# Optimization experiments

Measured on AMD Instinct MI355X. Metric: run time of the kernel, lower is better.

The kernel has to match this reference:

```python
import jax, jax.numpy as jnp
import numpy as np

HEADS = 4
KNN_K = 20
BN_EPS = 1e-5


def conv1x1(w, b, x):
    # 1x1 Conv1d: w [out, in], x [B, in, N] -> [B, out, N]
    return jnp.einsum('oc,bcn->bon', w, x) + b[None, :, None]


def setup_inputs() -> dict:
    key = jax.random.key(0)
    B, C, N = 2, 128, 2048
    ks = jax.random.split(key, 16)
    W = lambda k, o, i: jax.random.normal(k, (o, i), jnp.float32) * 0.05
    V = lambda k, o: jax.random.normal(k, (o,), jnp.float32) * 0.05
    return {
        'desc1': jax.random.normal(ks[0], (B, C, N, 1), jnp.float32),
        'wq': W(ks[1], C, C), 'bq': V(ks[2], C),
        'wk': W(ks[3], C, C), 'bk': V(ks[4], C),
        'wv': W(ks[5], C, C), 'bv': V(ks[6], C),
        'wm': W(ks[7], C, C), 'bm': V(ks[8], C),
        'w1': W(ks[9], 2 * C, 2 * C), 'b1': V(ks[10], 2 * C),
        'gamma': jnp.ones((2 * C,), jnp.float32),
        'beta': jnp.zeros((2 * C,), jnp.float32),
        'w2': W(ks[11], C, 2 * C), 'b2': V(ks[12], C),
    }


def reference(desc1, wq, bq, wk, bk, wv, bv, wm, bm, w1, b1, gamma, beta, w2, b2):
    x = desc1[..., 0]                      # [B, C, N]
    B, C, N = x.shape
    D = C // HEADS

    q = conv1x1(wq, bq, x).reshape(B, HEADS, D, N)
    k = conv1x1(wk, bk, x).reshape(B, HEADS, D, N)
    v = conv1x1(wv, bv, x).reshape(B, HEADS, D, N)

    # kNN on raw descriptors: pd = -||xi||^2 + 2 xi.xj - ||xj||^2 (larger = closer)
    xx = jnp.sum(x * x, axis=1)            # [B, N]
    pd = 2.0 * jnp.einsum('bcn,bcm->bnm', x, x) - xx[:, :, None] - xx[:, None, :]
    idx = jax.lax.top_k(pd, KNN_K)[1]      # [B, N, K]

    # scatter ones at kNN indices, then keep only mutual neighbors
    bI = jnp.arange(B)[:, None, None]
    nI = jnp.arange(N)[None, :, None]
    mask = jnp.zeros((B, N, N), x.dtype).at[bI, nI, idx].set(1.0)
    mask = mask * mask.transpose(0, 2, 1)  # [B, N, N]

    score = jnp.einsum('bhdn,bhdm->bhnm', q, k) / (D ** 0.5)
    m = mask[:, None]                      # broadcast over heads
    score = score * m + (-1e9) * (1.0 - m)
    score = jax.nn.softmax(score, axis=-1)

    av = jnp.einsum('bhnm,bhdm->bhdn', score, v).reshape(B, C, N)
    av = conv1x1(wm, bm, av)

    h = conv1x1(w1, b1, jnp.concatenate([x, av], axis=1))  # [B, 2C, N]
    mu = jnp.mean(h, axis=(0, 2), keepdims=True)
    var = jnp.var(h, axis=(0, 2), keepdims=True)           # biased, matches torch BN
    h = (h - mu) / jnp.sqrt(var + BN_EPS) * gamma[None, :, None] + beta[None, :, None]
    h = jax.nn.relu(h)

    out = x + conv1x1(w2, b2, h)
    return out[..., None]                  # [B, C, N, 1]
```

## Files before the change

### kernel.cpp

```cpp
#include <hip/hip_runtime.h>
#include <math.h>

#define NPT 2048
#define KNN 20

typedef const float* fp;
typedef __attribute__((ext_vector_type(4))) float f32x4;
typedef __attribute__((ext_vector_type(8))) short s16x8;

__device__ __forceinline__ ushort f2bf_rne(float v) {
    unsigned u = __float_as_uint(v);
    unsigned r = u + 0x7FFFu + ((u >> 16) & 1u);
    return (ushort)(r >> 16);
}
__device__ __forceinline__ float bfbits2f(ushort h) {
    return __uint_as_float(((unsigned)h) << 16);
}
__device__ __forceinline__ s16x8 ldfrag(const ushort* p) {
    union { uint4 u; s16x8 s; } cv;
    cv.u = *reinterpret_cast<const uint4*>(p);
    return cv.s;
}
__device__ __forceinline__ void f8_hilo(const float* row, s16x8* hi, s16x8* lo) {
    float4 f0 = *reinterpret_cast<const float4*>(row);
    float4 f1 = *reinterpret_cast<const float4*>(row + 4);
    float f[8] = {f0.x, f0.y, f0.z, f0.w, f1.x, f1.y, f1.z, f1.w};
    union { ushort u[8]; s16x8 s; } H, L;
    #pragma unroll
    for (int j = 0; j < 8; j++) {
        ushort h = f2bf_rne(f[j]);
        H.u[j] = h;
        L.u[j] = f2bf_rne(f[j] - bfbits2f(h));
    }
    *hi = H.s; *lo = L.s;
}

__global__ __launch_bounds__(256) void prep_all(
    fp xbf, fp wq, fp wk, fp wv, fp wm, fp w1, fp w2, fp bm, fp b1,
    float* xx, ushort* xhiF, ushort* xloF,
    ushort* wqFhi, ushort* wqFlo, ushort* wkFhi, ushort* wkFlo,
    ushort* wvFhi, ushort* wvFlo,
    ushort* wcFhi, ushort* wcFlo, ushort* w2Fhi, ushort* w2Flo,
    float* b1p, float* stats) {
    int t = threadIdx.x;
    if (blockIdx.x < 256) {
        __shared__ float xs[16][129];
        __shared__ float xpart[16][17];
        int p0 = blockIdx.x * 16;
        int b = p0 >> 11, n0 = p0 & 2047;
        fp xb = xbf + (size_t)b * 128 * NPT;
        {
            int c = t >> 1, half = t & 1;
            float4 f0 = *reinterpret_cast<const float4*>(xb + (size_t)c * NPT + n0 + half * 8);
            float4 f1 = *reinterpret_cast<const float4*>(xb + (size_t)c * NPT + n0 + half * 8 + 4);
            xs[half * 8 + 0][c] = f0.x; xs[half * 8 + 1][c] = f0.y;
            xs[half * 8 + 2][c] = f0.z; xs[half * 8 + 3][c] = f0.w;
            xs[half * 8 + 4][c] = f1.x; xs[half * 8 + 5][c] = f1.y;
            xs[half * 8 + 6][c] = f1.z; xs[half * 8 + 7][c] = f1.w;
        }
        __syncthreads();
        int p = t & 15, g = t >> 4, c0 = g * 8;
        float f[8];
        #pragma unroll
        for (int j = 0; j < 8; j++) f[j] = xs[p][c0 + j];
        float ps = 0.f;
        #pragma unroll
        for (int j = 0; j < 8; j++) ps += f[j] * f[j];
        xpart[p][g] = ps;
        union { ushort u[8]; uint4 q; } H, L;
        #pragma unroll
        for (int j = 0; j < 8; j++) {
            ushort hi = f2bf_rne(f[j]);
            H.u[j] = hi;
            L.u[j] = f2bf_rne(f[j] - bfbits2f(hi));
        }
        size_t off = ((size_t)blockIdx.x * 4 + (c0 >> 5)) * 512
                   + (size_t)(((((c0 >> 3) & 3) * 16) + p) * 8);
        *reinterpret_cast<uint4*>(xhiF + off) = H.q;
        *reinterpret_cast<uint4*>(xloF + off) = L.q;
        __syncthreads();
        if (t < 16) {
            float s = 0.f;
            #pragma unroll
            for (int gg = 0; gg < 16; gg++) s += xpart[t][gg];
            xx[p0 + t] = s;
        }
        return;
    }
    int wid = (blockIdx.x - 256) * 256 + t;
    if (wid < 49152) {
        int which = wid >> 14, e = wid & 16383;
        int lane = (e >> 3) & 63, j = e & 7, kk = (e >> 9) & 3, nt = e >> 11;
        int n = nt * 16 + (lane & 15);
        int k = kk * 32 + (lane >> 4) * 8 + j;
        fp src = which == 0 ? wq : which == 1 ? wk : wv;
        float v = src[n * 128 + k];
        ushort hi = f2bf_rne(v);
        (which == 0 ? wqFhi : which == 1 ? wkFhi : wvFhi)[e] = hi;
        (which == 0 ? wqFlo : which == 1 ? wkFlo : wvFlo)[e] = f2bf_rne(v - bfbits2f(hi));
    } else if (wid < 114688) {
        int e = wid - 49152;
        int j = e & 7, lane = (e >> 3) & 63, kk = (e >> 9) & 7, nt = e >> 12;
        int n = nt * 16 + (lane & 15);
        int k = kk * 32 + (lane >> 4) * 8 + j;
        float v;
        if (k < 128) {
            v = w1[n * 256 + k];
        } else {
            int c = k - 128;
            float s = 0.f;
            for (int i = 0; i < 128; i += 4) {
                float4 wr = *reinterpret_cast<const float4*>(w1 + n * 256 + 128 + i);
                s += wr.x * wm[(i + 0) * 128 + c];
                s += wr.y * wm[(i + 1) * 128 + c];
                s += wr.z * wm[(i + 2) * 128 + c];
                s += wr.w * wm[(i + 3) * 128 + c];
            }
            v = s;
        }
        ushort hi = f2bf_rne(v);
        wcFhi[e] = hi;
        wcFlo[e] = f2bf_rne(v - bfbits2f(hi));
    } else if (wid < 147456) {
        int e = wid - 114688;
        int j = e & 7, lane = (e >> 3) & 63, kk = (e >> 9) & 7, nt = e >> 12;
        int n = nt * 16 + (lane & 15);
        int k = kk * 32 + (lane >> 4) * 8 + j;
        float v = w2[n * 256 + k];
        ushort hi = f2bf_rne(v);
        w2Fhi[e] = hi;
        w2Flo[e] = f2bf_rne(v - bfbits2f(hi));
    } else if (wid < 147712) {
        int o = wid - 147456;
        float s = b1[o];
        for (int i = 0; i < 128; i++)
            s += w1[o * 256 + 128 + i] * bm[i];
        b1p[o] = s;
    } else {
        stats[wid - 147712] = 0.0f;
    }
}

#define MERGE(off) { float ov = __shfl_xor(bv, off); int oi = __shfl_xor(bi, off); \
                     if (ov > bv || (ov == bv && oi < bi)) { bv = ov; bi = oi; } }

__global__ __launch_bounds__(1024) void gemm_key_topk(
    const ushort* xhiF, const ushort* xloF, const float* xx,
    const ushort* wqFhi, const ushort* wqFlo,
    const ushort* wkFhi, const ushort* wkFlo,
    const ushort* wvFhi, const ushort* wvFlo,
    fp bq, fp bk, fp bv_, float* qT, float* kT, float* vT,
    int* idxbuf, float* scratch) {
    __shared__ float chm[16][64];
    __shared__ float sv[16][256];
    __shared__ int   si[16][256];
    __shared__ float Trow[16];
    __shared__ int   rowcnt[16];
    __shared__ int   ovfAll;
    int tt = threadIdx.x, w = tt >> 6, lane = tt & 63;
    int rt = blockIdx.x;
    int slab = rt >> 7, rtl = rt & 127;
    int cl = lane & 15, quad = lane >> 4;

    if (tt < 16) rowcnt[tt] = 0;
    if (tt == 16) ovfAll = 0;

    s16x8 ahi[4], alo[4];
    #pragma unroll
    for (int kk = 0; kk < 4; kk++) {
        ahi[kk] = ldfrag(xhiF + ((size_t)(rt * 4 + kk)) * 512 + lane * 8);
        alo[kk] = ldfrag(xloF + ((size_t)(rt * 4 + kk)) * 512 + lane * 8);
    }

    if (w < 12) {
        f32x4 acc[2];
        acc[0] = (f32x4){0.f, 0.f, 0.f, 0.f};
        acc[1] = (f32x4){0.f, 0.f, 0.f, 0.f};
        #pragma unroll
        for (int kk = 0; kk < 4; kk++) {
            #pragma unroll
            for (int i = 0; i < 2; i++) {
                int pair = w * 2 + i;
                int mat = pair >> 3, nt = pair & 7;
                const ushort* whi = mat == 0 ? wqFhi : mat == 1 ? wkFhi : wvFhi;
                const ushort* wlo = mat == 0 ? wqFlo : mat == 1 ? wkFlo : wvFlo;
                s16x8 bhi = ldfrag(whi + ((size_t)(nt * 4 + kk)) * 512 + lane * 8);
                s16x8 blo = ldfrag(wlo + ((size_t)(nt * 4 + kk)) * 512 + lane * 8);
                acc[i] = __builtin_amdgcn_mfma_f32_16x16x32_bf16(ahi[kk], bhi, acc[i], 0, 0, 0);
                acc[i] = __builtin_amdgcn_mfma_f32_16x16x32_bf16(alo[kk], bhi, acc[i], 0, 0, 0);
                acc[i] = __builtin_amdgcn_mfma_f32_16x16x32_bf16(ahi[kk], blo, acc[i], 0, 0, 0);
            }
        }
        int p0 = rt * 16;
        #pragma unroll
        for (int i = 0; i < 2; i++) {
            int pair = w * 2 + i;
            int mat = pair >> 3, nt = pair & 7;
            fp bias    = mat == 0 ? bq : mat == 1 ? bk : bv_;
            float* out = mat == 0 ? qT : mat == 1 ? kT : vT;
            int o = nt * 16 + cl;
            float bvv = bias[o];
            #pragma unroll
            for (int r = 0; r < 4; r++)
                out[(size_t)(p0 + quad * 4 + r) * 128 + o] = acc[i][r] + bvv;
        }
    }

    f32x4 key[8];
    #pragma unroll
    for (int c = 0; c < 8; c++) {
        int ctl = w * 8 + c;
        int ct = slab * 128 + ctl;
        f32x4 a = (f32x4){0.f, 0.f, 0.f, 0.f};
        #pragma unroll
        for (int kk = 0; kk < 4; kk++) {
            s16x8 bh = ldfrag(xhiF + ((size_t)(ct * 4 + kk)) * 512 + lane * 8);
            s16x8 bl = ldfrag(xloF + ((size_t)(ct * 4 + kk)) * 512 + lane * 8);
            a = __builtin_amdgcn_mfma_f32_16x16x32_bf16(ahi[kk], bh, a, 0, 0, 0);
            a = __builtin_amdgcn_mfma_f32_16x16x32_bf16(alo[kk], bh, a, 0, 0, 0);
            a = __builtin_amdgcn_mfma_f32_16x16x32_bf16(ahi[kk], bl, a, 0, 0, 0);
        }
        float xxc = xx[slab * 2048 + ctl * 16 + cl];
        #pragma unroll
        for (int r = 0; r < 4; r++) a[r] = 2.0f * a[r] - xxc;
        key[c] = a;
    }

    {
        float m[4];
        #pragma unroll
        for (int r = 0; r < 4; r++) {
            float mm = key[0][r];
            #pragma unroll
            for (int c = 1; c < 8; c++) mm = fmaxf(mm, key[c][r]);
            mm = fmaxf(mm, __shfl_xor(mm, 1));
            mm = fmaxf(mm, __shfl_xor(mm, 2));
            m[r] = mm;
        }
        if ((cl & 3) == 0) {
            #pragma unroll
            for (int r = 0; r < 4; r++)
                chm[quad * 4 + r][w * 4 + (cl >> 2)] = m[r];
        }
    }
    __syncthreads();

    {
        float bs = chm[w][lane];
        #pragma unroll
        for (int k = 2; k <= 64; k <<= 1) {
            #pragma unroll
            for (int j = k >> 1; j > 0; j >>= 1) {
                float o = __shfl_xor(bs, j);
                bool dirDesc = (lane & k) != 0;
                bool upper   = (lane & j) != 0;
                bs = (upper != dirDesc) ? fmaxf(bs, o) : fminf(bs, o);
            }
        }
        float T = __shfl(bs, 44);
        if (lane == 0) Trow[w] = T;
    }
    __syncthreads();

    #pragma unroll
    for (int r = 0; r < 4; r++) {
        int row = quad * 4 + r;
        float T = Trow[row];
        #pragma unroll
        for (int c = 0; c < 8; c++) {
            float v = key[c][r];
            if (v >= T) {
                int pos = atomicAdd(&rowcnt[row], 1);
                if (pos < 256) {
                    sv[row][pos] = v;
                    si[row][pos] = w * 128 + c * 16 + cl;
                }
            }
        }
    }
    __syncthreads();
    if (tt == 0) {
        int o = 0;
        for (int i = 0; i < 16; i++) o |= (rowcnt[i] > 256) ? 1 : 0;
        ovfAll = o;
    }
    __syncthreads();
    int ovf = ovfAll;

    int S = rowcnt[w];
    if (S <= 256) {
        float vl[4]; int il[4];
        #pragma unroll
        for (int s = 0; s < 4; s++) {
            int g = lane + s * 64;
            bool ok = g < S;
            vl[s] = ok ? sv[w][g] : -3.4e38f;
            il[s] = ok ? si[w][g] : 0x7FFFFFFF;
        }
        unsigned removed = 0u;
        for (int iter = 0; iter < KNN; iter++) {
            float bv = -3.4e38f; int bi = 0x7FFFFFFF;
            #pragma unroll
            for (int s = 0; s < 4; s++) {
                bool live = ((removed >> s) & 1u) == 0u;
                if (live && (vl[s] > bv || (vl[s] == bv && il[s] < bi))) {
                    bv = vl[s]; bi = il[s];
                }
            }
            MERGE(32) MERGE(16) MERGE(8) MERGE(4) MERGE(2) MERGE(1)
            if (lane == 0)
                idxbuf[(size_t)(slab * 2048 + rtl * 16 + w) * KNN + iter] = bi & 2047;
            #pragma unroll
            for (int s = 0; s < 4; s++)
                if (il[s] == bi) removed |= 1u << s;
        }
    }

    if (ovf) {
        #pragma unroll
        for (int c = 0; c < 8; c++)
            #pragma unroll
            for (int r = 0; r < 4; r++)
                scratch[((size_t)rt * 16 + quad * 4 + r) * 2048 + w * 128 + c * 16 + cl]
                    = key[c][r];
        __syncthreads();
        if (rowcnt[w] > 256) {
            const float* rowp = scratch + ((size_t)rt * 16 + w) * 2048;
            float rv[32];
            #pragma unroll
            for (int j = 0; j < 32; j++) rv[j] = rowp[j * 64 + lane];
            unsigned removed = 0u;
            for (int iter = 0; iter < KNN; iter++) {
                float bv = -3.4e38f; int bi = 0;
                #pragma unroll
                for (int sl = 0; sl < 32; sl++) {
                    bool live = ((removed >> sl) & 1u) == 0u;
                    if (live && rv[sl] > bv) { bv = rv[sl]; bi = sl * 64 + lane; }
                }
                MERGE(32) MERGE(16) MERGE(8) MERGE(4) MERGE(2) MERGE(1)
                if (lane == 0)
                    idxbuf[(size_t)(slab * 2048 + rtl * 16 + w) * KNN + iter] = bi;
                if ((bi & 63) == lane) removed |= 1u << (bi >> 6);
            }
        }
    }
}

__global__ __launch_bounds__(256) void k3_attn(
    fp qT, fp kT, fp vT, const int* idxbuf, float* avT) {
    __shared__ float sbuf[2][KNN * 4];
    __shared__ int   mlist[2][KNN];
    __shared__ int   cnt_s[2];
    int tt = threadIdx.x;
    int half = tt >> 7, t = tt & 127;
    int p = blockIdx.x * 2 + half;
    int b = p >> 11, n = p & 2047;
    int bbase = b * NPT;
    int h = t >> 5;

    if ((tt >> 6) == half * 2) {
        int lane = tt & 63;
        bool fl = false; int m = 0;
        if (lane < KNN) {
            m = idxbuf[(size_t)p * KNN + lane] & 2047;
            const int4* mrow = reinterpret_cast<const int4*>(idxbuf + (size_t)(bbase + m) * KNN);
            int4 r0 = mrow[0], r1 = mrow[1], r2 = mrow[2], r3 = mrow[3], r4 = mrow[4];
            fl = (r0.x == n) || (r0.y == n) || (r0.z == n) || (r0.w == n)
              || (r1.x == n) || (r1.y == n) || (r1.z == n) || (r1.w == n)
              || (r2.x == n) || (r2.y == n) || (r2.z == n) || (r2.w == n)
              || (r3.x == n) || (r3.y == n) || (r3.z == n) || (r3.w == n)
              || (r4.x == n) || (r4.y == n) || (r4.z == n) || (r4.w == n);
        }
        unsigned long long mask = __ballot(fl);
        int pos = __popcll(mask & ((1ull << lane) - 1ull));
        if (fl) mlist[half][pos] = m;
        if (lane == 0) cnt_s[half] = (int)__popcll(mask);
    }
    __syncthreads();

    int cnt = cnt_s[half];
    float qv = qT[(size_t)p * 128 + t];
    for (int jj = 0; jj < cnt; jj++) {
        int m = mlist[half][jj];
        float prod = qv * kT[(size_t)(bbase + m) * 128 + t];
        prod += __shfl_xor(prod, 16);
        prod += __shfl_xor(prod, 8);
        prod += __shfl_xor(prod, 4);
        prod += __shfl_xor(prod, 2);
        prod += __shfl_xor(prod, 1);
        if ((t & 31) == 0) sbuf[half][jj * 4 + h] = prod * 0.17677669529663687f;
    }
    __syncthreads();

    float mx = -3.4e38f;
    for (int j = 0; j < cnt; j++) mx = fmaxf(mx, sbuf[half][j * 4 + h]);
    float den = 0.f;
    for (int j = 0; j < cnt; j++) den += expf(sbuf[half][j * 4 + h] - mx);
    float inv = (cnt > 0) ? (1.0f / den) : 0.0f;
    float acc = 0.f;
    for (int j = 0; j < cnt; j++) {
        float pw = expf(sbuf[half][j * 4 + h] - mx) * inv;
        acc += pw * vT[(size_t)(bbase + mlist[half][j]) * 128 + t];
    }
    avT[(size_t)p * 128 + t] = acc;
}

__global__ __launch_bounds__(256) void k4b_h(
    const ushort* xhiF, const ushort* xloF, const float* avT,
    const ushort* wcFhi, const ushort* wcFlo,
    const float* b1p, float* hbuf, float* stats) {
    int t = threadIdx.x, cs = t >> 6, lane = t & 63;
    int rt = blockIdx.x;
    int p0 = rt * 16;

    f32x4 acc[4];
    #pragma unroll
    for (int j = 0; j < 4; j++) acc[j] = (f32x4){0.f, 0.f, 0.f, 0.f};

    for (int kk = 0; kk < 8; kk++) {
        s16x8 ahi, alo;
        if (kk < 4) {
            ahi = ldfrag(xhiF + ((size_t)(rt * 4 + kk)) * 512 + lane * 8);
            alo = ldfrag(xloF + ((size_t)(rt * 4 + kk)) * 512 + lane * 8);
        } else {
            const float* arow = avT + (size_t)(p0 + (lane & 15)) * 128
                              + (kk - 4) * 32 + (lane >> 4) * 8;
            f8_hilo(arow, &ahi, &alo);
        }
        #pragma unroll
        for (int j = 0; j < 4; j++) {
            int nt = cs * 4 + j;
            s16x8 bhi = ldfrag(wcFhi + ((size_t)(nt * 8 + kk)) * 512 + lane * 8);
            s16x8 blo = ldfrag(wcFlo + ((size_t)(nt * 8 + kk)) * 512 + lane * 8);
            acc[j] = __builtin_amdgcn_mfma_f32_16x16x32_bf16(ahi, bhi, acc[j], 0, 0, 0);
            acc[j] = __builtin_amdgcn_mfma_f32_16x16x32_bf16(alo, bhi, acc[j], 0, 0, 0);
            acc[j] = __builtin_amdgcn_mfma_f32_16x16x32_bf16(ahi, blo, acc[j], 0, 0, 0);
        }
    }

    int cl = lane & 15, quad = lane >> 4;
    #pragma unroll
    for (int j = 0; j < 4; j++) {
        int o = cs * 64 + j * 16 + cl;
        float bb = b1p[o];
        float s = 0.f, s2 = 0.f;
        #pragma unroll
        for (int r = 0; r < 4; r++) {
            float v = acc[j][r] + bb;
            hbuf[(size_t)(p0 + quad * 4 + r) * 256 + o] = v;
            s += v; s2 += v * v;
        }
        s  += __shfl_xor(s, 16);  s  += __shfl_xor(s, 32);
        s2 += __shfl_xor(s2, 16); s2 += __shfl_xor(s2, 32);
        if (quad == 0) {
            atomicAdd(&stats[o], s);
            atomicAdd(&stats[256 + o], s2);
        }
    }
}

__global__ __launch_bounds__(256) void k5b_out(
    const float* hbuf, const float* stats, fp gamma, fp beta,
    const ushort* w2Fhi, const ushort* w2Flo,
    fp b2, fp xbf, float* out) {
    int t = threadIdx.x, wvi = t >> 6, lane = t & 63;
    int rt = blockIdx.x;
    int p0 = rt * 16;

    f32x4 acc[2];
    acc[0] = (f32x4){0.f, 0.f, 0.f, 0.f};
    acc[1] = (f32x4){0.f, 0.f, 0.f, 0.f};

    for (int kk = 0; kk < 8; kk++) {
        int c0 = kk * 32 + (lane >> 4) * 8;
        const float* hrow = hbuf + (size_t)(p0 + (lane & 15)) * 256 + c0;
        float4 f0 = *reinterpret_cast<const float4*>(hrow);
        float4 f1 = *reinterpret_cast<const float4*>(hrow + 4);
        float4 s0 = *reinterpret_cast<const float4*>(stats + c0);
        float4 s1 = *reinterpret_cast<const float4*>(stats + c0 + 4);
        float4 q0 = *reinterpret_cast<const float4*>(stats + 256 + c0);
        float4 q1 = *reinterpret_cast<const float4*>(stats + 256 + c0 + 4);
        float4 g0 = *reinterpret_cast<const float4*>(gamma + c0);
        float4 g1 = *reinterpret_cast<const float4*>(gamma + c0 + 4);
        float4 e0 = *reinterpret_cast<const float4*>(beta + c0);
        float4 e1 = *reinterpret_cast<const float4*>(beta + c0 + 4);
        float f[8] = {f0.x, f0.y, f0.z, f0.w, f1.x, f1.y, f1.z, f1.w};
        float sm[8] = {s0.x, s0.y, s0.z, s0.w, s1.x, s1.y, s1.z, s1.w};
        float sq[8] = {q0.x, q0.y, q0.z, q0.w, q1.x, q1.y, q1.z, q1.w};
        float gm[8] = {g0.x, g0.y, g0.z, g0.w, g1.x, g1.y, g1.z, g1.w};
        float bt[8] = {e0.x, e0.y, e0.z, e0.w, e1.x, e1.y, e1.z, e1.w};
        union { ushort u[8]; s16x8 s; } H, L;
        #pragma unroll
        for (int j = 0; j < 8; j++) {
            float mu  = sm[j] * (1.0f / 4096.0f);
            float var = fmaxf(sq[j] * (1.0f / 4096.0f) - mu * mu, 0.0f);
            float a    = gm[j] / sqrtf(var + 1e-5f);
            float cadd = bt[j] - mu * a;
            float v = fmaxf(f[j] * a + cadd, 0.0f);
            ushort hi = f2bf_rne(v);
            H.u[j] = hi;
            L.u[j] = f2bf_rne(v - bfbits2f(hi));
        }
        s16x8 ahi = H.s, alo = L.s;
        #pragma unroll
        for (int jj = 0; jj < 2; jj++) {
            int nt = wvi * 2 + jj;
            s16x8 bhi = ldfrag(w2Fhi + ((size_t)(nt * 8 + kk)) * 512 + lane * 8);
            s16x8 blo = ldfrag(w2Flo + ((size_t)(nt * 8 + kk)) * 512 + lane * 8);
            acc[jj] = __builtin_amdgcn_mfma_f32_16x16x32_bf16(ahi, bhi, acc[jj], 0, 0, 0);
            acc[jj] = __builtin_amdgcn_mfma_f32_16x16x32_bf16(alo, bhi, acc[jj], 0, 0, 0);
            acc[jj] = __builtin_amdgcn_mfma_f32_16x16x32_bf16(ahi, blo, acc[jj], 0, 0, 0);
        }
    }
    int cl = lane & 15, quad = lane >> 4;
    int b = p0 >> 11, n0 = p0 & 2047;
    #pragma unroll
    for (int jj = 0; jj < 2; jj++) {
        int o = (wvi * 2 + jj) * 16 + cl;
        float bb = b2[o];
        size_t base = (size_t)b * 128 * NPT + (size_t)o * NPT + n0 + quad * 4;
        float4 xv = *reinterpret_cast<const float4*>(xbf + base);
        float4 ov;
        ov.x = acc[jj][0] + bb + xv.x;
        ov.y = acc[jj][1] + bb + xv.y;
        ov.z = acc[jj][2] + bb + xv.z;
        ov.w = acc[jj][3] + bb + xv.w;
        *reinterpret_cast<float4*>(out + base) = ov;
    }
}

#define WS_FULL 44978176u

extern "C" void kernel_launch(void* const* d_in, const int* in_sizes, int n_in,
                              void* d_out, int out_size, void* d_ws, size_t ws_size,
                              hipStream_t stream) {
    fp desc1 = (fp)d_in[0];
    fp wq = (fp)d_in[1];  fp bq = (fp)d_in[2];
    fp wk = (fp)d_in[3];  fp bk = (fp)d_in[4];
    fp wv = (fp)d_in[5];  fp bv = (fp)d_in[6];
    fp wm = (fp)d_in[7];  fp bm = (fp)d_in[8];
    fp w1 = (fp)d_in[9];  fp b1 = (fp)d_in[10];
    fp gamma = (fp)d_in[11]; fp beta = (fp)d_in[12];
    fp w2 = (fp)d_in[13]; fp b2 = (fp)d_in[14];

    if (ws_size < (size_t)WS_FULL) return;

    char* ws = (char*)d_ws;
    float*  qT    = (float*) (ws + 0);
    float*  kT    = (float*) (ws + 2097152);
    float*  vT    = (float*) (ws + 4194304);
    float*  avT   = (float*) (ws + 6291456);
    float*  xx    = (float*) (ws + 8388608);
    int*    idxb  = (int*)   (ws + 8404992);
    float*  stats = (float*) (ws + 8732672);
    float*  b1p   = (float*) (ws + 8734720);
    ushort* wqFhi = (ushort*)(ws + 8736768);
    ushort* wqFlo = (ushort*)(ws + 8769536);
    ushort* wkFhi = (ushort*)(ws + 8802304);
    ushort* wkFlo = (ushort*)(ws + 8835072);
    ushort* wvFhi = (ushort*)(ws + 8867840);
    ushort* wvFlo = (ushort*)(ws + 8900608);
    ushort* wcFhi = (ushort*)(ws + 8933376);
    ushort* wcFlo = (ushort*)(ws + 9064448);
    ushort* w2Fhi = (ushort*)(ws + 9195520);
    ushort* w2Flo = (ushort*)(ws + 9261056);
    ushort* xhiF  = (ushort*)(ws + 9326592);
    ushort* xloF  = (ushort*)(ws + 10375168);
    float*  scratch = (float*)(ws + 11423744);
    float*  hbuf  = (float*) (ws + 0);

    prep_all<<<835, 256, 0, stream>>>(desc1, wq, wk, wv, wm, w1, w2, bm, b1,
                                      xx, xhiF, xloF,
                                      wqFhi, wqFlo, wkFhi, wkFlo, wvFhi, wvFlo,
                                      wcFhi, wcFlo, w2Fhi, w2Flo, b1p, stats);
    gemm_key_topk<<<256, 1024, 0, stream>>>(xhiF, xloF, xx,
                                            wqFhi, wqFlo, wkFhi, wkFlo,
                                            wvFhi, wvFlo,
                                            bq, bk, bv, qT, kT, vT, idxb,
                                            scratch);
    k3_attn<<<2048, 256, 0, stream>>>(qT, kT, vT, idxb, avT);
    k4b_h<<<256, 256, 0, stream>>>(xhiF, xloF, avT, wcFhi, wcFlo,
                                   b1p, hbuf, stats);
    k5b_out<<<256, 256, 0, stream>>>(hbuf, stats, gamma, beta, w2Fhi, w2Flo,
                                     b2, desc1, (float*)d_out);
}
```

Measured before the change: 187.0 us.

## Split kNN top-k columns across two blocks and merge partial lists

Measured after the change: 236.5 us. 26.4% more time.

```diff
diff --git a/kernel.cpp b/kernel.cpp
--- a/kernel.cpp
+++ b/kernel.cpp
@@ -144,26 +144,25 @@
 #define MERGE(off) { float ov = __shfl_xor(bv, off); int oi = __shfl_xor(bi, off); \
                      if (ov > bv || (ov == bv && oi < bi)) { bv = ov; bi = oi; } }
 
-__global__ __launch_bounds__(1024) void gemm_key_topk(
+__global__ __launch_bounds__(1024, 8) void gemm_key_topk(
     const ushort* xhiF, const ushort* xloF, const float* xx,
     const ushort* wqFhi, const ushort* wqFlo,
     const ushort* wkFhi, const ushort* wkFlo,
     const ushort* wvFhi, const ushort* wvFlo,
     fp bq, fp bk, fp bv_, float* qT, float* kT, float* vT,
-    int* idxbuf, float* scratch) {
-    __shared__ float chm[16][64];
+    float* pv, int* pi, float* scratch) {
+    __shared__ float chm[16][32];
     __shared__ float sv[16][256];
     __shared__ int   si[16][256];
     __shared__ float Trow[16];
     __shared__ int   rowcnt[16];
     __shared__ int   ovfAll;
     int tt = threadIdx.x, w = tt >> 6, lane = tt & 63;
-    int rt = blockIdx.x;
+    int rt = blockIdx.x >> 1, half = blockIdx.x & 1;
     int slab = rt >> 7, rtl = rt & 127;
     int cl = lane & 15, quad = lane >> 4;
 
     if (tt < 16) rowcnt[tt] = 0;
-    if (tt == 16) ovfAll = 0;
 
     s16x8 ahi[4], alo[4];
     #pragma unroll
@@ -172,7 +171,7 @@
         alo[kk] = ldfrag(xloF + ((size_t)(rt * 4 + kk)) * 512 + lane * 8);
     }
 
-    if (w < 12) {
+    if (half == 0 && w < 12) {
         f32x4 acc[2];
         acc[0] = (f32x4){0.f, 0.f, 0.f, 0.f};
         acc[1] = (f32x4){0.f, 0.f, 0.f, 0.f};
@@ -206,10 +205,10 @@
         }
     }
 
-    f32x4 key[8];
-    #pragma unroll
-    for (int c = 0; c < 8; c++) {
-        int ctl = w * 8 + c;
+    f32x4 key[4];
+    #pragma unroll
+    for (int c = 0; c < 4; c++) {
+        int ctl = half * 64 + w * 4 + c;
         int ct = slab * 128 + ctl;
         f32x4 a = (f32x4){0.f, 0.f, 0.f, 0.f};
         #pragma unroll
@@ -232,21 +231,22 @@
         for (int r = 0; r < 4; r++) {
             float mm = key[0][r];
             #pragma unroll
-            for (int c = 1; c < 8; c++) mm = fmaxf(mm, key[c][r]);
+            for (int c = 1; c < 4; c++) mm = fmaxf(mm, key[c][r]);
             mm = fmaxf(mm, __shfl_xor(mm, 1));
             mm = fmaxf(mm, __shfl_xor(mm, 2));
+            mm = fmaxf(mm, __shfl_xor(mm, 4));
             m[r] = mm;
         }
-        if ((cl & 3) == 0) {
+        if ((cl & 7) == 0) {
             #pragma unroll
             for (int r = 0; r < 4; r++)
-                chm[quad * 4 + r][w * 4 + (cl >> 2)] = m[r];
+                chm[quad * 4 + r][w * 2 + (cl >> 3)] = m[r];
         }
     }
     __syncthreads();
 
     {
-        float bs = chm[w][lane];
+        float bs = (lane < 32) ? chm[w][lane] : -3.4e38f;
         #pragma unroll
         for (int k = 2; k <= 64; k <<= 1) {
             #pragma unroll
@@ -267,13 +267,13 @@
         int row = quad * 4 + r;
         float T = Trow[row];
         #pragma unroll
-        for (int c = 0; c < 8; c++) {
+        for (int c = 0; c < 4; c++) {
             float v = key[c][r];
             if (v >= T) {
                 int pos = atomicAdd(&rowcnt[row], 1);
                 if (pos < 256) {
                     sv[row][pos] = v;
-                    si[row][pos] = w * 128 + c * 16 + cl;
+                    si[row][pos] = (half * 64 + w * 4 + c) * 16 + cl;
                 }
             }
         }
@@ -288,6 +288,7 @@
     int ovf = ovfAll;
 
     int S = rowcnt[w];
+    size_t obase = ((size_t)(slab * 2048 + rtl * 16 + w) * 2 + half) * KNN;
     if (S <= 256) {
         float vl[4]; int il[4];
         #pragma unroll
@@ -308,8 +309,7 @@
                 }
             }
             MERGE(32) MERGE(16) MERGE(8) MERGE(4) MERGE(2) MERGE(1)
-            if (lane == 0)
-                idxbuf[(size_t)(slab * 2048 + rtl * 16 + w) * KNN + iter] = bi & 2047;
+            if (lane == 0) { pv[obase + iter] = bv; pi[obase + iter] = bi & 2047; }
             #pragma unroll
             for (int s = 0; s < 4; s++)
                 if (il[s] == bi) removed |= 1u << s;
@@ -318,31 +318,48 @@
 
     if (ovf) {
         #pragma unroll
-        for (int c = 0; c < 8; c++)
+        for (int c = 0; c < 4; c++)
             #pragma unroll
             for (int r = 0; r < 4; r++)
-                scratch[((size_t)rt * 16 + quad * 4 + r) * 2048 + w * 128 + c * 16 + cl]
-                    = key[c][r];
+                scratch[((size_t)rt * 16 + quad * 4 + r) * 2048
+                        + (half * 64 + w * 4 + c) * 16 + cl] = key[c][r];
         __syncthreads();
         if (rowcnt[w] > 256) {
-            const float* rowp = scratch + ((size_t)rt * 16 + w) * 2048;
-            float rv[32];
-            #pragma unroll
-            for (int j = 0; j < 32; j++) rv[j] = rowp[j * 64 + lane];
+            const float* rowp = scratch + ((size_t)rt * 16 + w) * 2048 + half * 1024;
+            float rv[16];
+            #pragma unroll
+            for (int j = 0; j < 16; j++) rv[j] = rowp[j * 64 + lane];
             unsigned removed = 0u;
             for (int iter = 0; iter < KNN; iter++) {
                 float bv = -3.4e38f; int bi = 0;
                 #pragma unroll
-                for (int sl = 0; sl < 32; sl++) {
+                for (int sl = 0; sl < 16; sl++) {
                     bool live = ((removed >> sl) & 1u) == 0u;
-                    if (live && rv[sl] > bv) { bv = rv[sl]; bi = sl * 64 + lane; }
+                    if (live && rv[sl] > bv) {
+                        bv = rv[sl]; bi = half * 1024 + sl * 64 + lane;
+                    }
                 }
                 MERGE(32) MERGE(16) MERGE(8) MERGE(4) MERGE(2) MERGE(1)
-                if (lane == 0)
-                    idxbuf[(size_t)(slab * 2048 + rtl * 16 + w) * KNN + iter] = bi;
-                if ((bi & 63) == lane) removed |= 1u << (bi >> 6);
+                if (lane == 0) { pv[obase + iter] = bv; pi[obase + iter] = bi; }
+                if ((bi & 63) == lane) removed |= 1u << ((bi - half * 1024) >> 6);
             }
         }
+    }
+}
+
+__global__ __launch_bounds__(256) void merge_topk(
+    const float* pv, const int* pi, int* idxbuf) {
+    int row = blockIdx.x * 256 + threadIdx.x;
+    const float* va = pv + (size_t)row * 2 * KNN;
+    const int*   ia = pi + (size_t)row * 2 * KNN;
+    int a = 0, b = KNN;
+    #pragma unroll
+    for (int i = 0; i < KNN; i++) {
+        float x = va[a], y = va[b];
+        int ix = ia[a], iy = ia[b];
+        bool ta = (x > y) || (x == y && ix < iy);
+        idxbuf[(size_t)row * KNN + i] = ta ? ix : iy;
+        if (ta) a++; else b++;
     }
 }
 
@@ -529,7 +546,7 @@
     }
 }
 
-#define WS_FULL 44978176u
+#define WS_FULL 46288896u
 
 extern "C" void kernel_launch(void* const* d_in, const int* in_sizes, int n_in,
                               void* d_out, int out_size, void* d_ws, size_t ws_size,
@@ -566,18 +583,21 @@
     ushort* w2Flo = (ushort*)(ws + 9261056);
     ushort* xhiF  = (ushort*)(ws + 9326592);
     ushort* xloF  = (ushort*)(ws + 10375168);
-    float*  scratch = (float*)(ws + 11423744);
+    float*  pv    = (float*) (ws + 11423744);
+    int*    pi    = (int*)   (ws + 12079104);
+    float*  scratch = (float*)(ws + 12734464);
     float*  hbuf  = (float*) (ws + 0);
 
     prep_all<<<835, 256, 0, stream>>>(desc1, wq, wk, wv, wm, w1, w2, bm, b1,
                                       xx, xhiF, xloF,
                                       wqFhi, wqFlo, wkFhi, wkFlo, wvFhi, wvFlo,
                                       wcFhi, wcFlo, w2Fhi, w2Flo, b1p, stats);
-    gemm_key_topk<<<256, 1024, 0, stream>>>(xhiF, xloF, xx,
+    gemm_key_topk<<<512, 1024, 0, stream>>>(xhiF, xloF, xx,
                                             wqFhi, wqFlo, wkFhi, wkFlo,
                                             wvFhi, wvFlo,
-                                            bq, bk, bv, qT, kT, vT, idxb,
-                                            scratch);
+                                            bq, bk, bv, qT, kT, vT,
+                                            pv, pi, scratch);
+    merge_topk<<<16, 256, 0, stream>>>(pv, pi, idxb);
     k3_attn<<<2048, 256, 0, stream>>>(qT, kT, vT, idxb, avT);
     k4b_h<<<256, 256, 0, stream>>>(xhiF, xloF, avT, wcFhi, wcFlo,
                                    b1p, hbuf, stats);
```
